# Kernel tuning notes

Measured on AMD Instinct MI355X. Metric: run time of the kernel, lower is better.

Reference implementation:

```python
import jax, jax.numpy as jnp
import numpy as np

B, T = 4096, 32            # batch, max_length (time steps)
ADIM, ODIM = 64, 64        # raw action / obs dims
HID = 128                  # encoder hidden units
EA, EO = 16, 16            # encoded action / obs dims
R = 32                     # MPO rank
OUT = 8                    # output_dim (last core's trailing dim)


def setup_inputs() -> dict:
    key = jax.random.key(0)
    ks = jax.random.split(key, 12)
    s = lambda k, shape: jax.random.normal(k, shape, jnp.float32) * 0.1
    return dict(
        action=jax.random.normal(ks[0], (B, T, ADIM), jnp.float32),
        obs=jax.random.normal(ks[1], (B, T, ODIM), jnp.float32),
        # encoder_action: Linear(ADIM,HID) -> Linear(HID,EA), no activation
        Wa0=s(ks[2], (ADIM, HID)), ba0=jnp.zeros((HID,), jnp.float32),
        Wa1=s(ks[3], (HID, EA)),   ba1=jnp.zeros((EA,), jnp.float32),
        # encoder_obs: Linear(ODIM,HID) -> Linear(HID,EO), no activation
        Wo0=s(ks[4], (ODIM, HID)), bo0=jnp.zeros((HID,), jnp.float32),
        Wo1=s(ks[5], (HID, EO)),   bo1=jnp.zeros((EO,), jnp.float32),
        # MPO / tensor-train cores: first has left bond 1, last has right bond OUT
        H_first=s(ks[6], (1, EA, EO, R)),
        H_mid=s(ks[7], (T - 2, R, EA, EO, R)),
        H_last=s(ks[8], (R, EA, EO, OUT)),
    )


def reference(action, obs, Wa0, ba0, Wa1, ba1, Wo0, bo0, Wo1, bo1,
              H_first, H_mid, H_last):
    # FC encoders (stacked linears, no nonlinearity), applied per (b, t)
    a = (action @ Wa0 + ba0) @ Wa1 + ba1   # [B, T, EA]
    o = (obs @ Wo0 + bo0) @ Wo1 + bo1      # [B, T, EO]

    # per-timestep contracted cores: einsum('pjkl,ij,ik->pil')
    # t = 0: left bond p == 1, drop it -> carry [B, R]
    c0 = jnp.einsum('jkl,bj,bk->bl', H_first[0], a[:, 0], o[:, 0])
    # middle steps, all at once: [T-2, R, B, R]
    mids = jnp.einsum('tpjkl,btj,btk->tpbl', H_mid, a[:, 1:-1], o[:, 1:-1])
    # last step: [R, B, OUT]
    last = jnp.einsum('pjkl,bj,bk->pbl', H_last, a[:, -1], o[:, -1])

    # sequential chain contraction einsum('pil,lik->pik') with p == 1
    def step(c, core):  # c: [B, R], core: [R, B, R]
        return jnp.einsum('bl,lbk->bk', c, core), None

    c, _ = jax.lax.scan(step, c0, mids)
    out = jnp.einsum('bl,lbk->bk', c, last)  # [B, OUT] (== squeeze of [1,B,OUT])
    return out
```

## Files before the change

### kernel.cpp

```cpp
#include <hip/hip_runtime.h>

#define B_    4096
#define T_    32
#define OUT_  8
#define BTILE 32

typedef _Float16 f16;
typedef _Float16 f16x4 __attribute__((ext_vector_type(4)));
typedef _Float16 f16x8 __attribute__((ext_vector_type(8)));
typedef float    f32x4 __attribute__((ext_vector_type(4)));

#define MFMA16(a, b, c) __builtin_amdgcn_mfma_f32_16x16x32_f16((a), (b), (c), 0, 0, 0)

#define WS_AENC 16384u
#define WS_OENC (WS_AENC + 4194304u)
#define WS_H    (WS_OENC + 4194304u)
#define WS_U    (WS_H + 16842752u)
#define WS_FLAG (WS_U + 524288u)

#define BSTR 1064
#define KGRP 264
#define WSZ  (32 * BSTR)

__global__ void k_fuse_w(const float* __restrict__ Wa0, const float* __restrict__ ba0,
                         const float* __restrict__ Wa1, const float* __restrict__ ba1,
                         const float* __restrict__ Wo0, const float* __restrict__ bo0,
                         const float* __restrict__ Wo1, const float* __restrict__ bo1,
                         float* __restrict__ ws) {
  const int tid = threadIdx.x;
  for (int idx = tid; idx < 1024; idx += 256) {
    const int d = idx >> 4, j = idx & 15;
    float s = 0.f, s2 = 0.f;
    for (int h = 0; h < 128; ++h) {
      s  += Wa0[d * 128 + h] * Wa1[h * 16 + j];
      s2 += Wo0[d * 128 + h] * Wo1[h * 16 + j];
    }
    ws[idx] = s;
    ws[1024 + idx] = s2;
  }
  if (tid < 16) {
    float s = 0.f, s2 = 0.f;
    for (int h = 0; h < 128; ++h) {
      s  += ba0[h] * Wa1[h * 16 + tid];
      s2 += bo0[h] * Wo1[h * 16 + tid];
    }
    ws[2048 + tid] = s + ba1[tid];
    ws[2112 + tid] = s2 + bo1[tid];
  }
}

__global__ void k_encode(const float* __restrict__ action, const float* __restrict__ obs,
                         const float* __restrict__ ws,
                         f16* __restrict__ aenc, f16* __restrict__ oenc) {
  const int tid = threadIdx.x;
  const int lane = tid & 63;
  const int v = tid >> 6;
  const int m16 = lane & 15, g4 = lane >> 4;
  const int bt0 = blockIdx.x * 64 + v * 16;

  f16x8 wbA[2], wbB[2];
  #pragma unroll
  for (int ks = 0; ks < 2; ++ks)
    #pragma unroll
    for (int h = 0; h < 2; ++h)
      #pragma unroll
      for (int r = 0; r < 4; ++r) {
        const int d = ks * 32 + h * 16 + g4 * 4 + r;
        wbA[ks][h * 4 + r] = (f16)ws[d * 16 + m16];
        wbB[ks][h * 4 + r] = (f16)ws[1024 + d * 16 + m16];
      }
  const float biasA = ws[2048 + m16], biasB = ws[2112 + m16];
  f32x4 accA = {biasA, biasA, biasA, biasA};
  f32x4 accB = {biasB, biasB, biasB, biasB};

  const float* ar = action + (size_t)(bt0 + m16) * 64;
  const float* br = obs    + (size_t)(bt0 + m16) * 64;
  #pragma unroll
  for (int ks = 0; ks < 2; ++ks) {
    f16x8 aa, oo;
    #pragma unroll
    for (int h = 0; h < 2; ++h) {
      const f32x4 a4 = *(const f32x4*)(ar + ks * 32 + h * 16 + g4 * 4);
      const f32x4 o4 = *(const f32x4*)(br + ks * 32 + h * 16 + g4 * 4);
      #pragma unroll
      for (int r = 0; r < 4; ++r) { aa[h * 4 + r] = (f16)a4[r]; oo[h * 4 + r] = (f16)o4[r]; }
    }
    accA = MFMA16(aa, wbA[ks], accA);
    accB = MFMA16(oo, wbB[ks], accB);
  }
  #pragma unroll
  for (int r = 0; r < 4; ++r) {
    aenc[(size_t)(bt0 + g4 * 4 + r) * 16 + m16] = (f16)accA[r];
    oenc[(size_t)(bt0 + g4 * 4 + r) * 16 + m16] = (f16)accB[r];
  }
}

__global__ void k_hprep(const float* __restrict__ Hf, const float* __restrict__ Hm,
                        const float* __restrict__ Hl, f16* __restrict__ hdst) {
  const int x = blockIdx.x * 256 + threadIdx.x;
  const int lane = x & 63;
  const int gid = x >> 6;
  const int nf = gid & 1, s = (gid >> 1) & 7, p = (gid >> 4) & 31, t = gid >> 9;
  const int m16 = lane & 15, g4 = lane >> 4;
  const int l = nf * 16 + m16;
  f16x8 gout;
  #pragma unroll
  for (int h = 0; h < 2; ++h) {
    const int j = 2 * s + h;
    #pragma unroll
    for (int r = 0; r < 4; ++r) {
      const int kk = g4 * 4 + r;
      float vsrc;
      if (t == 0)       vsrc = (p == 0) ? Hf[(j * 16 + kk) * 32 + l] : 0.f;
      else if (t == 31) vsrc = (l < 8) ? Hl[((p * 16 + j) * 16 + kk) * 8 + l] : 0.f;
      else              vsrc = Hm[((((size_t)(t - 1) * 32 + p) * 16 + j) * 16 + kk) * 32 + l];
      gout[h * 4 + r] = (f16)(vsrc * 0.125f);
    }
  }
  *(f16x8*)((char*)hdst + (size_t)x * 16) = gout;
}

__launch_bounds__(512)
__global__ void k_main(const f16* __restrict__ aenc, const f16* __restrict__ oenc,
                       const char* __restrict__ hws, float* __restrict__ uex,
                       int* __restrict__ flag, float* __restrict__ out) {
  __shared__ __align__(16) f16 Wl[WSZ];
  __shared__ __align__(16) f16 Ml[WSZ];
  __shared__ float u_lds[1024];

  const int tid  = threadIdx.x;
  const int lane = tid & 63;
  const int w    = tid >> 6;
  const int m16  = lane & 15;
  const int g4   = lane >> 4;
  const int bt   = blockIdx.x >> 1;
  const int g    = blockIdx.x & 1;
  const int b0   = bt * BTILE;
  const int t0   = g * 16;

  const f16* ap0 = aenc + ((size_t)(b0 + m16) * T_ + t0) * 16;
  const f16* ap1 = aenc + ((size_t)(b0 + 16 + m16) * T_ + t0) * 16;
  f16x8 aL0 = *(const f16x8*)ap0, aH0 = *(const f16x8*)(ap0 + 8);
  f16x8 aL1 = *(const f16x8*)ap1, aH1 = *(const f16x8*)(ap1 + 8);
  f16x4 ovA = *(const f16x4*)(oenc + ((size_t)(b0 + m16) * T_ + t0) * 16 + g4 * 4);
  f16x4 ovB = *(const f16x4*)(oenc + ((size_t)(b0 + 16 + m16) * T_ + t0) * 16 + g4 * 4);

  const char* hl = hws + (size_t)lane * 16;
  const f32x4 zz = {0.f, 0.f, 0.f, 0.f};

  f16x8 bufA[8], bufB[8];
  {
    const char* ga = hl + (size_t)((t0 * 32 + 4 * w) * 16) * 1024;
    #pragma unroll
    for (int i = 0; i < 8; ++i) bufA[i] = *(const f16x8*)(ga + i * 1024);
  }

  #pragma clang loop unroll(disable)
  for (int tau = 0; tau < 16; ++tau) {
    const int t = t0 + tau;
    f16x8 efr0[8], efr1[8];
    #pragma unroll
    for (int sl = 0; sl < 8; ++sl) {
      const f16 a00 = (sl < 4) ? aL0[2 * sl]     : aH0[2 * sl - 8];
      const f16 a01 = (sl < 4) ? aL0[2 * sl + 1] : aH0[2 * sl - 7];
      const f16 a10 = (sl < 4) ? aL1[2 * sl]     : aH1[2 * sl - 8];
      const f16 a11 = (sl < 4) ? aL1[2 * sl + 1] : aH1[2 * sl - 7];
      #pragma unroll
      for (int r = 0; r < 4; ++r) {
        efr0[sl][r] = a00 * ovA[r]; efr0[sl][4 + r] = a01 * ovA[r];
        efr1[sl][r] = a10 * ovB[r]; efr1[sl][4 + r] = a11 * ovB[r];
      }
    }
    const int tn = (tau < 15) ? t + 1 : t;
    {
      const f16* an0 = aenc + ((size_t)(b0 + m16) * T_ + tn) * 16;
      const f16* an1 = aenc + ((size_t)(b0 + 16 + m16) * T_ + tn) * 16;
      aL0 = *(const f16x8*)an0; aH0 = *(const f16x8*)(an0 + 8);
      aL1 = *(const f16x8*)an1; aH1 = *(const f16x8*)(an1 + 8);
      ovA = *(const f16x4*)(oenc + ((size_t)(b0 + m16) * T_ + tn) * 16 + g4 * 4);
      ovB = *(const f16x4*)(oenc + ((size_t)(b0 + 16 + m16) * T_ + tn) * 16 + g4 * 4);
    }

    f32x4 acc[4][2][2];
    #pragma unroll
    for (int pp = 0; pp < 4; ++pp) {
      const int p = 4 * w + pp;
      acc[pp][0][0] = zz; acc[pp][0][1] = zz; acc[pp][1][0] = zz; acc[pp][1][1] = zz;
      {
        const char* gb = hl + ((size_t)((t * 32 + p) * 16) + 8) * 1024;
        #pragma unroll
        for (int i = 0; i < 8; ++i) bufB[i] = *(const f16x8*)(gb + i * 1024);
      }
      __builtin_amdgcn_s_setprio(1);
      #pragma unroll
      for (int sl = 0; sl < 4; ++sl) {
        acc[pp][0][0] = MFMA16(efr0[sl], bufA[sl * 2 + 0], acc[pp][0][0]);
        acc[pp][1][0] = MFMA16(efr1[sl], bufA[sl * 2 + 0], acc[pp][1][0]);
        acc[pp][0][1] = MFMA16(efr0[sl], bufA[sl * 2 + 1], acc[pp][0][1]);
        acc[pp][1][1] = MFMA16(efr1[sl], bufA[sl * 2 + 1], acc[pp][1][1]);
      }
      __builtin_amdgcn_s_setprio(0);
      {
        const int pnext = (pp < 3) ? p + 1 : 4 * w;
        const int tnext = (pp < 3) ? t : tn;
        const char* ga = hl + (size_t)((tnext * 32 + pnext) * 16) * 1024;
        #pragma unroll
        for (int i = 0; i < 8; ++i) bufA[i] = *(const f16x8*)(ga + i * 1024);
      }
      __builtin_amdgcn_s_setprio(1);
      #pragma unroll
      for (int sl = 4; sl < 8; ++sl) {
        acc[pp][0][0] = MFMA16(efr0[sl], bufB[(sl - 4) * 2 + 0], acc[pp][0][0]);
        acc[pp][1][0] = MFMA16(efr1[sl], bufB[(sl - 4) * 2 + 0], acc[pp][1][0]);
        acc[pp][0][1] = MFMA16(efr0[sl], bufB[(sl - 4) * 2 + 1], acc[pp][0][1]);
        acc[pp][1][1] = MFMA16(efr1[sl], bufB[(sl - 4) * 2 + 1], acc[pp][1][1]);
      }
      __builtin_amdgcn_s_setprio(0);
    }

    #pragma unroll
    for (int mf = 0; mf < 2; ++mf)
      #pragma unroll
      for (int nf = 0; nf < 2; ++nf)
        #pragma unroll
        for (int r = 0; r < 4; ++r) {
          const int b = mf * 16 + g4 * 4 + r;
          const int n = nf * 16 + m16;
          f16x4 v;
          v[0] = (f16)acc[0][mf][nf][r];
          v[1] = (f16)acc[1][mf][nf][r];
          v[2] = (f16)acc[2][mf][nf][r];
          v[3] = (f16)acc[3][mf][nf][r];
          *(f16x4*)&Ml[b * BSTR + (w & 3) * KGRP + n * 8 + (w >> 2) * 4] = v;
        }
    asm volatile("s_waitcnt lgkmcnt(0)" ::: "memory");
    __builtin_amdgcn_s_barrier();

    if (tau == 0) {
      #pragma unroll
      for (int rep = 0; rep < 64; ++rep) {
        const int e = tid + rep * 512;
        const int b = e >> 10, k = (e >> 5) & 31, rho = e & 31;
        Wl[b * BSTR + ((k >> 2) & 3) * KGRP + rho * 8 + (k >> 4) * 4 + (k & 3)] =
          Ml[b * BSTR + ((rho >> 2) & 3) * KGRP + k * 8 + (rho >> 4) * 4 + (rho & 3)];
      }
      asm volatile("s_waitcnt lgkmcnt(0)" ::: "memory");
      __builtin_amdgcn_s_barrier();
    } else {
      f32x4 n00[4], n01[4], n10[4], n11[4];
      #pragma unroll
      for (int bb = 0; bb < 4; ++bb) {
        const int bx = (4 * w + bb) * BSTR + g4 * KGRP;
        const f16x8 A0 = *(const f16x8*)&Wl[bx + m16 * 8];
        const f16x8 A1 = *(const f16x8*)&Wl[bx + (16 + m16) * 8];
        const f16x8 B0 = *(const f16x8*)&Ml[bx + m16 * 8];
        const f16x8 B1 = *(const f16x8*)&Ml[bx + (16 + m16) * 8];
        n00[bb] = MFMA16(A0, B0, zz);
        n01[bb] = MFMA16(A0, B1, zz);
        n10[bb] = MFMA16(A1, B0, zz);
        n11[bb] = MFMA16(A1, B1, zz);
      }
      __builtin_amdgcn_s_barrier();
      #pragma unroll
      for (int bb = 0; bb < 4; ++bb) {
        const int bx = (4 * w + bb) * BSTR + (m16 >> 2) * KGRP + (m16 & 3);
        #pragma unroll
        for (int rr = 0; rr < 4; ++rr) {
          const int pA = (g4 * 4 + rr) * 8, pB = (16 + g4 * 4 + rr) * 8;
          Wl[bx + pA]     = (f16)n00[bb][rr];
          Wl[bx + pA + 4] = (f16)n01[bb][rr];
          Wl[bx + pB]     = (f16)n10[bb][rr];
          Wl[bx + pB + 4] = (f16)n11[bb][rr];
        }
      }
    }
  }

  asm volatile("s_waitcnt lgkmcnt(0)" ::: "memory");
  __builtin_amdgcn_s_barrier();

  if (g == 0) {
    #pragma unroll
    for (int rep = 0; rep < 2; ++rep) {
      const int e = tid + rep * 512;
      const int bb = e >> 5, m = e & 31;
      const float v = (float)Wl[bb * BSTR + ((m >> 2) & 3) * KGRP + (m >> 4) * 4 + (m & 3)];
      __hip_atomic_store(uex + bt * 1024 + e, v, __ATOMIC_RELAXED, __HIP_MEMORY_SCOPE_AGENT);
    }
    __syncthreads();
    if (tid == 0)
      __hip_atomic_store(flag + bt, 1, __ATOMIC_RELEASE, __HIP_MEMORY_SCOPE_AGENT);
  } else {
    if (tid == 0) {
      while (__hip_atomic_load(flag + bt, __ATOMIC_ACQUIRE, __HIP_MEMORY_SCOPE_AGENT) == 0)
        __builtin_amdgcn_s_sleep(16);
    }
    __syncthreads();
    #pragma unroll
    for (int rep = 0; rep < 2; ++rep) {
      const int e = tid + rep * 512;
      u_lds[e] = __hip_atomic_load(uex + bt * 1024 + e, __ATOMIC_RELAXED, __HIP_MEMORY_SCOPE_AGENT);
    }
    __syncthreads();
    if (tid < 256) {
      const int bb = tid >> 3, o = tid & 7;
      float s = 0.f;
      #pragma unroll
      for (int rho = 0; rho < 32; ++rho)
        s += u_lds[bb * 32 + rho] *
             (float)Wl[bb * BSTR + (o >> 2) * KGRP + rho * 8 + (o & 3)];
      out[(size_t)(b0 + bb) * OUT_ + o] = s * 0x1p96f;
    }
  }
}

extern "C" void kernel_launch(void* const* d_in, const int* in_sizes, int n_in,
                              void* d_out, int out_size, void* d_ws, size_t ws_size,
                              hipStream_t stream) {
  (void)in_sizes; (void)n_in; (void)out_size; (void)ws_size;
  const float* action = (const float*)d_in[0];
  const float* obs    = (const float*)d_in[1];
  const float* Wa0 = (const float*)d_in[2];
  const float* ba0 = (const float*)d_in[3];
  const float* Wa1 = (const float*)d_in[4];
  const float* ba1 = (const float*)d_in[5];
  const float* Wo0 = (const float*)d_in[6];
  const float* bo0 = (const float*)d_in[7];
  const float* Wo1 = (const float*)d_in[8];
  const float* bo1 = (const float*)d_in[9];
  const float* Hf  = (const float*)d_in[10];
  const float* Hm  = (const float*)d_in[11];
  const float* Hl  = (const float*)d_in[12];
  char*  ws  = (char*)d_ws;
  float* out = (float*)d_out;

  k_fuse_w<<<1, 256, 0, stream>>>(Wa0, ba0, Wa1, ba1, Wo0, bo0, Wo1, bo1, (float*)ws);
  k_encode<<<(B_ * T_) / 64, 256, 0, stream>>>(action, obs, (const float*)ws,
                                               (f16*)(ws + WS_AENC), (f16*)(ws + WS_OENC));
  k_hprep<<<4096, 256, 0, stream>>>(Hf, Hm, Hl, (f16*)(ws + WS_H));
  hipMemsetAsync(ws + WS_FLAG, 0, 512, stream);
  k_main<<<256, 512, 0, stream>>>((const f16*)(ws + WS_AENC), (const f16*)(ws + WS_OENC),
                                  (const char*)(ws + WS_H), (float*)(ws + WS_U),
                                  (int*)(ws + WS_FLAG), out);
}
```

Baseline: 180.7 us.

## Restructure core-fragment streaming with 4-deep register ring and on-the-fly A fragments

```diff
diff --git a/kernel.cpp b/kernel.cpp
--- a/kernel.cpp
+++ b/kernel.cpp
@@ -6,6 +6,7 @@
 #define BTILE 32
 
 typedef _Float16 f16;
+typedef _Float16 f16x2 __attribute__((ext_vector_type(2)));
 typedef _Float16 f16x4 __attribute__((ext_vector_type(4)));
 typedef _Float16 f16x8 __attribute__((ext_vector_type(8)));
 typedef float    f32x4 __attribute__((ext_vector_type(4)));
@@ -121,6 +122,7 @@
 }
 
 __launch_bounds__(512)
+__attribute__((amdgpu_waves_per_eu(2, 2)))
 __global__ void k_main(const f16* __restrict__ aenc, const f16* __restrict__ oenc,
                        const char* __restrict__ hws, float* __restrict__ uex,
                        int* __restrict__ flag, float* __restrict__ out) {
@@ -148,30 +150,84 @@
   const char* hl = hws + (size_t)lane * 16;
   const f32x4 zz = {0.f, 0.f, 0.f, 0.f};
 
-  f16x8 bufA[8], bufB[8];
-  {
-    const char* ga = hl + (size_t)((t0 * 32 + 4 * w) * 16) * 1024;
-    #pragma unroll
-    for (int i = 0; i < 8; ++i) bufA[i] = *(const f16x8*)(ga + i * 1024);
-  }
+  f16x8 u0[8], u1[8], u2[8], u3[8];
+
+#define ULOAD(U, TT, QQ) do {                                                  \
+    const char* ga_ = hl + (size_t)((((TT) * 32 + 4 * w + ((QQ) >> 1)) * 16    \
+                                    + ((QQ) & 1) * 8)) * 1024;                 \
+    _Pragma("unroll")                                                          \
+    for (int i_ = 0; i_ < 8; ++i_) U[i_] = *(const f16x8*)(ga_ + i_ * 1024);   \
+  } while (0)
+
+#define UCOMP(U, ACC, H) do {                                                  \
+    __builtin_amdgcn_s_setprio(1);                                             \
+    _Pragma("unroll")                                                          \
+    for (int s2_ = 0; s2_ < 4; ++s2_) {                                        \
+      const int sl_ = 4 * (H) + s2_;                                           \
+      const f16 a00 = (sl_ < 4) ? aL0[2 * sl_]     : aH0[2 * sl_ - 8];         \
+      const f16 a01 = (sl_ < 4) ? aL0[2 * sl_ + 1] : aH0[2 * sl_ - 7];         \
+      const f16 a10 = (sl_ < 4) ? aL1[2 * sl_]     : aH1[2 * sl_ - 8];         \
+      const f16 a11 = (sl_ < 4) ? aL1[2 * sl_ + 1] : aH1[2 * sl_ - 7];         \
+      f16x8 af0, af1;                                                          \
+      _Pragma("unroll")                                                        \
+      for (int r_ = 0; r_ < 4; ++r_) {                                         \
+        af0[r_] = a00 * ovA[r_]; af0[4 + r_] = a01 * ovA[r_];                  \
+        af1[r_] = a10 * ovB[r_]; af1[4 + r_] = a11 * ovB[r_];                  \
+      }                                                                        \
+      ACC[0][0] = MFMA16(af0, U[2 * s2_],     ACC[0][0]);                      \
+      ACC[0][1] = MFMA16(af0, U[2 * s2_ + 1], ACC[0][1]);                      \
+      ACC[1][0] = MFMA16(af1, U[2 * s2_],     ACC[1][0]);                      \
+      ACC[1][1] = MFMA16(af1, U[2 * s2_ + 1], ACC[1][1]);                      \
+    }                                                                          \
+    __builtin_amdgcn_s_setprio(0);                                             \
+  } while (0)
+
+#define MSTORE(OFF) do {                                                       \
+    _Pragma("unroll")                                                          \
+    for (int mf_ = 0; mf_ < 2; ++mf_)                                          \
+      _Pragma("unroll")                                                        \
+      for (int nf_ = 0; nf_ < 2; ++nf_)                                        \
+        _Pragma("unroll")                                                      \
+        for (int r_ = 0; r_ < 4; ++r_) {                                       \
+          const int b_ = mf_ * 16 + g4 * 4 + r_;                               \
+          const int n_ = nf_ * 16 + m16;                                       \
+          f16x2 v_;                                                            \
+          v_[0] = (f16)accP0[mf_][nf_][r_];                                    \
+          v_[1] = (f16)accP1[mf_][nf_][r_];                                    \
+          *(f16x2*)((char*)Ml + 2 * (b_ * BSTR + (w & 3) * KGRP + n_ * 8       \
+                                     + (w >> 2) * 4) + (OFF)) = v_;            \
+        }                                                                      \
+  } while (0)
+
+  ULOAD(u0, t0, 0);
+  ULOAD(u1, t0, 1);
 
   #pragma clang loop unroll(disable)
   for (int tau = 0; tau < 16; ++tau) {
     const int t = t0 + tau;
-    f16x8 efr0[8], efr1[8];
-    #pragma unroll
-    for (int sl = 0; sl < 8; ++sl) {
-      const f16 a00 = (sl < 4) ? aL0[2 * sl]     : aH0[2 * sl - 8];
-      const f16 a01 = (sl < 4) ? aL0[2 * sl + 1] : aH0[2 * sl - 7];
-      const f16 a10 = (sl < 4) ? aL1[2 * sl]     : aH1[2 * sl - 8];
-      const f16 a11 = (sl < 4) ? aL1[2 * sl + 1] : aH1[2 * sl - 7];
-      #pragma unroll
-      for (int r = 0; r < 4; ++r) {
-        efr0[sl][r] = a00 * ovA[r]; efr0[sl][4 + r] = a01 * ovA[r];
-        efr1[sl][r] = a10 * ovB[r]; efr1[sl][4 + r] = a11 * ovB[r];
-      }
-    }
     const int tn = (tau < 15) ? t + 1 : t;
+
+    f32x4 accP0[2][2], accP1[2][2];
+    #pragma unroll
+    for (int mf = 0; mf < 2; ++mf)
+      #pragma unroll
+      for (int nf = 0; nf < 2; ++nf) { accP0[mf][nf] = zz; accP1[mf][nf] = zz; }
+
+    ULOAD(u2, t, 2);  UCOMP(u0, accP0, 0);
+    ULOAD(u3, t, 3);  UCOMP(u1, accP0, 1);
+    ULOAD(u0, t, 4);  UCOMP(u2, accP1, 0);
+    ULOAD(u1, t, 5);  UCOMP(u3, accP1, 1);
+    MSTORE(0);
+    #pragma unroll
+    for (int mf = 0; mf < 2; ++mf)
+      #pragma unroll
+      for (int nf = 0; nf < 2; ++nf) { accP0[mf][nf] = zz; accP1[mf][nf] = zz; }
+    ULOAD(u2, t, 6);   UCOMP(u0, accP0, 0);
+    ULOAD(u3, t, 7);   UCOMP(u1, accP0, 1);
+    ULOAD(u0, tn, 0);  UCOMP(u2, accP1, 0);
+    ULOAD(u1, tn, 1);  UCOMP(u3, accP1, 1);
+    MSTORE(4);
+
     {
       const f16* an0 = aenc + ((size_t)(b0 + m16) * T_ + tn) * 16;
       const f16* an1 = aenc + ((size_t)(b0 + 16 + m16) * T_ + tn) * 16;
@@ -181,58 +237,6 @@
       ovB = *(const f16x4*)(oenc + ((size_t)(b0 + 16 + m16) * T_ + tn) * 16 + g4 * 4);
     }
 
-    f32x4 acc[4][2][2];
-    #pragma unroll
-    for (int pp = 0; pp < 4; ++pp) {
-      const int p = 4 * w + pp;
-      acc[pp][0][0] = zz; acc[pp][0][1] = zz; acc[pp][1][0] = zz; acc[pp][1][1] = zz;
-      {
-        const char* gb = hl + ((size_t)((t * 32 + p) * 16) + 8) * 1024;
-        #pragma unroll
-        for (int i = 0; i < 8; ++i) bufB[i] = *(const f16x8*)(gb + i * 1024);
-      }
-      __builtin_amdgcn_s_setprio(1);
-      #pragma unroll
-      for (int sl = 0; sl < 4; ++sl) {
-        acc[pp][0][0] = MFMA16(efr0[sl], bufA[sl * 2 + 0], acc[pp][0][0]);
-        acc[pp][1][0] = MFMA16(efr1[sl], bufA[sl * 2 + 0], acc[pp][1][0]);
-        acc[pp][0][1] = MFMA16(efr0[sl], bufA[sl * 2 + 1], acc[pp][0][1]);
-        acc[pp][1][1] = MFMA16(efr1[sl], bufA[sl * 2 + 1], acc[pp][1][1]);
-      }
-      __builtin_amdgcn_s_setprio(0);
-      {
-        const int pnext = (pp < 3) ? p + 1 : 4 * w;
-        const int tnext = (pp < 3) ? t : tn;
-        const char* ga = hl + (size_t)((tnext * 32 + pnext) * 16) * 1024;
-        #pragma unroll
-        for (int i = 0; i < 8; ++i) bufA[i] = *(const f16x8*)(ga + i * 1024);
-      }
-      __builtin_amdgcn_s_setprio(1);
-      #pragma unroll
-      for (int sl = 4; sl < 8; ++sl) {
-        acc[pp][0][0] = MFMA16(efr0[sl], bufB[(sl - 4) * 2 + 0], acc[pp][0][0]);
-        acc[pp][1][0] = MFMA16(efr1[sl], bufB[(sl - 4) * 2 + 0], acc[pp][1][0]);
-        acc[pp][0][1] = MFMA16(efr0[sl], bufB[(sl - 4) * 2 + 1], acc[pp][0][1]);
-        acc[pp][1][1] = MFMA16(efr1[sl], bufB[(sl - 4) * 2 + 1], acc[pp][1][1]);
-      }
-      __builtin_amdgcn_s_setprio(0);
-    }
-
-    #pragma unroll
-    for (int mf = 0; mf < 2; ++mf)
-      #pragma unroll
-      for (int nf = 0; nf < 2; ++nf)
-        #pragma unroll
-        for (int r = 0; r < 4; ++r) {
-          const int b = mf * 16 + g4 * 4 + r;
-          const int n = nf * 16 + m16;
-          f16x4 v;
-          v[0] = (f16)acc[0][mf][nf][r];
-          v[1] = (f16)acc[1][mf][nf][r];
-          v[2] = (f16)acc[2][mf][nf][r];
-          v[3] = (f16)acc[3][mf][nf][r];
-          *(f16x4*)&Ml[b * BSTR + (w & 3) * KGRP + n * 8 + (w >> 2) * 4] = v;
-        }
     asm volatile("s_waitcnt lgkmcnt(0)" ::: "memory");
     __builtin_amdgcn_s_barrier();
 
@@ -312,6 +316,9 @@
       out[(size_t)(b0 + bb) * OUT_ + o] = s * 0x1p96f;
     }
   }
+#undef ULOAD
+#undef UCOMP
+#undef MSTORE
 }
 
 extern "C" void kernel_launch(void* const* d_in, const int* in_sizes, int n_in,
```

New measurement: 175.5 us. 1.03x faster.
